# Performance work log

Hardware: AMD Instinct MI355X
Metric: run time of the kernel (lower is better)

The kernel has to match this reference:

```python
import jax, jax.numpy as jnp
import numpy as np

N, B, LMAX, DIM, IMG_DIM, LY, H = 32768, 16, 2560, 512, 768, 256, 8


def _layernorm(x, g, b, eps=1e-5):
    mu = jnp.mean(x, axis=-1, keepdims=True)
    var = jnp.mean(jnp.square(x - mu), axis=-1, keepdims=True)
    return (x - mu) * jax.lax.rsqrt(var + eps) * g + b


def setup_inputs() -> dict:
    key = jax.random.key(0)
    ks = jax.random.split(key, 16)
    s = DIM ** -0.5
    # ragged per-batch counts summing to N, all <= LMAX
    counts = np.full(B, N // B, dtype=np.int64)
    counts[: B // 2] += 200
    counts[B // 2:] -= 200
    batch_ids = jnp.asarray(np.repeat(np.arange(B), counts), dtype=jnp.int32)
    return {
        "F": jax.random.normal(ks[0], (N, DIM), jnp.float32),
        "y": jax.random.normal(ks[1], (B, LY, IMG_DIM), jnp.float32),
        "ln_g": jnp.ones((DIM,), jnp.float32),
        "ln_b": jnp.zeros((DIM,), jnp.float32),
        "Wq": jax.random.normal(ks[2], (DIM, DIM), jnp.float32) * s,
        "Wk": jax.random.normal(ks[3], (DIM, DIM), jnp.float32) * s,
        "Wv": jax.random.normal(ks[4], (DIM, DIM), jnp.float32) * s,
        "bq": jnp.zeros((DIM,), jnp.float32),
        "bk": jnp.zeros((DIM,), jnp.float32),
        "bv": jnp.zeros((DIM,), jnp.float32),
        "Wo": jax.random.normal(ks[5], (DIM, DIM), jnp.float32) * s,
        "bo": jnp.zeros((DIM,), jnp.float32),
        "W1": jax.random.normal(ks[6], (DIM, IMG_DIM), jnp.float32) * (IMG_DIM ** -0.5),
        "b1": jnp.zeros((DIM,), jnp.float32),
        "W2": jax.random.normal(ks[7], (DIM, DIM), jnp.float32) * s,
        "b2": jnp.zeros((DIM,), jnp.float32),
        "batch_ids": batch_ids,
        "Lmax": LMAX,
    }


def reference(F, y, ln_g, ln_b, Wq, Wk, Wv, bq, bk, bv, Wo, bo, W1, b1, W2, b2, batch_ids, Lmax):
    Bb, Ly, _ = y.shape
    n, dim = F.shape
    dh = dim // H
    # sparse -> dense: per-token slot index within its batch (batch_ids sorted)
    offsets = jnp.searchsorted(batch_ids, jnp.arange(Bb, dtype=batch_ids.dtype))
    pos = jnp.arange(n, dtype=jnp.int32) - offsets[batch_ids].astype(jnp.int32)
    xd = jnp.zeros((Bb, Lmax, dim), F.dtype).at[batch_ids, pos].set(F)  # [B,Lmax,D]
    # NOTE: self.norm is re-bound in subclass => same LayerNorm used twice
    xd = _layernorm(xd, ln_g, ln_b)
    # MLP fuse of image features: Linear -> GELU(exact) -> Linear
    ym = jax.nn.gelu(y @ W1.T + b1, approximate=False) @ W2.T + b2  # [B,Ly,D]
    # MHA cross-attention (no key_padding_mask: mask arg defaults to None)
    q = (xd @ Wq.T + bq).reshape(Bb, Lmax, H, dh)
    k = (ym @ Wk.T + bk).reshape(Bb, Ly, H, dh)
    v = (ym @ Wv.T + bv).reshape(Bb, Ly, H, dh)
    scores = jnp.einsum("bqhd,bkhd->bhqk", q, k) * (dh ** -0.5)
    attn = jax.nn.softmax(scores, axis=-1)
    o = jnp.einsum("bhqk,bkhd->bqhd", attn, v).reshape(Bb, Lmax, dim)
    o = o @ Wo.T + bo
    out_dense = _layernorm(xd + o, ln_g, ln_b)
    # dense -> sparse gather (equivalent to x_dense[x_mask])
    return out_dense[batch_ids, pos]
```

## Files before the change

### kernel.cpp

```cpp
#include <hip/hip_runtime.h>
#include <stdint.h>

#define NTOK 32768
#define BD   512
#define NB   16
#define LYK  256
#define IMGD 768

typedef __attribute__((ext_vector_type(4))) float f32x4;
typedef __attribute__((ext_vector_type(8))) short s16x8;
typedef __attribute__((ext_vector_type(4))) unsigned short u16x4;
typedef unsigned short u16;

__device__ __forceinline__ float bf2f(u16 u) {
  union { uint32_t i; float f; } v; v.i = ((uint32_t)u) << 16; return v.f;
}
__device__ __forceinline__ u16 f2bf(float f) {
  union { float f; uint32_t i; } v; v.f = f;
  uint32_t r = v.i + 0x7fffu + ((v.i >> 16) & 1u);
  return (u16)(r >> 16);
}
__device__ __forceinline__ u16 f2bf_fast(float f) {
  union { float f; uint32_t i; } v; v.f = f;
  return (u16)((v.i + 0x8000u) >> 16);
}
__device__ __forceinline__ void gl_lds16(const u16* g, u16* l) {
  __builtin_amdgcn_global_load_lds(
      (const __attribute__((address_space(1))) uint32_t*)g,
      (__attribute__((address_space(3))) uint32_t*)l, 16, 0, 0);
}
__device__ __forceinline__ f32x4 mfma16(s16x8 a, s16x8 b, f32x4 c) {
  return __builtin_amdgcn_mfma_f32_16x16x32_bf16(a, b, c, 0, 0, 0);
}

__global__ __launch_bounds__(256) void prep(
    const float* __restrict__ wq, const float* __restrict__ wk,
    const float* __restrict__ wv, const float* __restrict__ wo,
    const float* __restrict__ w2, const float* __restrict__ w1,
    const float* __restrict__ y,  const float* __restrict__ F,
    const float* __restrict__ g,  const float* __restrict__ be,
    const int* __restrict__ bids,
    u16* __restrict__ dq, u16* __restrict__ dkv, u16* __restrict__ dwo,
    u16* __restrict__ dw2, u16* __restrict__ dw1, u16* __restrict__ dy,
    u16* __restrict__ xn, int* __restrict__ off) {
  const int bid = blockIdx.x;
  if (bid < 2368) {
    const float* s; u16* d; int base;
    if      (bid < 128)  { s = wq; d = dq;            base = 0;   }
    else if (bid < 256)  { s = wk; d = dkv;           base = 128; }
    else if (bid < 384)  { s = wv; d = dkv + 262144;  base = 256; }
    else if (bid < 512)  { s = wo; d = dwo;           base = 384; }
    else if (bid < 640)  { s = w2; d = dw2;           base = 512; }
    else if (bid < 832)  { s = w1; d = dw1;           base = 640; }
    else                 { s = y;  d = dy;            base = 832; }
    int i = ((bid - base) * 256 + threadIdx.x) * 8;
    f32x4 a = *(const f32x4*)(s + i);
    f32x4 b = *(const f32x4*)(s + i + 4);
    s16x8 o;
#pragma unroll
    for (int j = 0; j < 4; ++j) { o[j] = (short)f2bf(a[j]); o[4 + j] = (short)f2bf(b[j]); }
    *(s16x8*)(d + i) = o;
  } else if (bid < 10560) {
    const int lane = threadIdx.x & 63;
    const size_t row = (size_t)(bid - 2368) * 4 + (threadIdx.x >> 6);
    const float* x = F + row * BD + lane * 8;
    f32x4 a = *(const f32x4*)x;
    f32x4 b = *(const f32x4*)(x + 4);
    float v[8] = {a[0], a[1], a[2], a[3], b[0], b[1], b[2], b[3]};
    float s = 0.f, s2 = 0.f;
#pragma unroll
    for (int j = 0; j < 8; ++j) { s += v[j]; s2 += v[j] * v[j]; }
#pragma unroll
    for (int m = 1; m < 64; m <<= 1) { s += __shfl_xor(s, m); s2 += __shfl_xor(s2, m); }
    float mean = s * (1.f / BD);
    float rstd = rsqrtf(s2 * (1.f / BD) - mean * mean + 1e-5f);
    const float* gp = g + lane * 8;
    const float* bp = be + lane * 8;
    s16x8 o;
#pragma unroll
    for (int j = 0; j < 8; ++j) o[j] = (short)f2bf((v[j] - mean) * rstd * gp[j] + bp[j]);
    *(s16x8*)(xn + row * BD + lane * 8) = o;
  } else {
    int b = threadIdx.x;
    if (b > NB) return;
    int lo = 0, hi = NTOK;
    while (lo < hi) { int mid = (lo + hi) >> 1; if (bids[mid] < b) lo = mid + 1; else hi = mid; }
    off[b] = lo;
  }
}

__global__ __launch_bounds__(256) void ln_bf16_f32(const u16* __restrict__ Z,
                                                   const float* __restrict__ g,
                                                   const float* __restrict__ be,
                                                   float* __restrict__ out) {
  const int lane = threadIdx.x & 63;
  const size_t row = (size_t)blockIdx.x * 4 + (threadIdx.x >> 6);
  s16x8 zv = *(const s16x8*)(Z + row * BD + lane * 8);
  float v[8];
#pragma unroll
  for (int j = 0; j < 8; ++j) v[j] = bf2f((u16)zv[j]);
  float s = 0.f, s2 = 0.f;
#pragma unroll
  for (int j = 0; j < 8; ++j) { s += v[j]; s2 += v[j] * v[j]; }
#pragma unroll
  for (int m = 1; m < 64; m <<= 1) { s += __shfl_xor(s, m); s2 += __shfl_xor(s2, m); }
  float mean = s * (1.f / BD);
  float rstd = rsqrtf(s2 * (1.f / BD) - mean * mean + 1e-5f);
  const float* gp = g + lane * 8;
  const float* bp = be + lane * 8;
  f32x4 o0, o1;
#pragma unroll
  for (int j = 0; j < 4; ++j) o0[j] = (v[j] - mean) * rstd * gp[j] + bp[j];
#pragma unroll
  for (int j = 0; j < 4; ++j) o1[j] = (v[4 + j] - mean) * rstd * gp[4 + j] + bp[4 + j];
  float* op = out + row * BD + lane * 8;
  *(f32x4*)op = o0;
  *(f32x4*)(op + 4) = o1;
}

template <int EPI>
__global__ __launch_bounds__(256, 2) void gemm64(const u16* __restrict__ A,
                                                 const u16* __restrict__ W,
                                                 const float* __restrict__ bias,
                                                 u16* __restrict__ C, int K) {
  __shared__ u16 As[64 * 32];
  __shared__ u16 Bs[128 * 32];
  const int tid = threadIdx.x;
  const int wave = tid >> 6, lane = tid & 63;
  const int wn = wave * 32;
  const int quad = lane >> 4, l16 = lane & 15;
  const int m0 = blockIdx.x * 64, n0 = blockIdx.y * 128;

  f32x4 acc[4][2];
#pragma unroll
  for (int i = 0; i < 4; ++i)
#pragma unroll
    for (int j = 0; j < 2; ++j) acc[i][j] = f32x4{0.f, 0.f, 0.f, 0.f};

  const int scol = (lane & 3) * 8;
  const u16* gA0 = A + (size_t)(m0 + wave * 16 + (lane >> 2)) * K + scol;
  const u16* gW0 = W + (size_t)(n0 + wave * 32 + (lane >> 2)) * K + scol;
  const u16* gW1 = gW0 + (size_t)16 * K;
  u16* lA = As + wave * 512;
  u16* lB = Bs + wave * 1024;

  for (int k0 = 0; k0 < K; k0 += 32) {
    __syncthreads();
    gl_lds16(gA0 + k0, lA);
    gl_lds16(gW0 + k0, lB);
    gl_lds16(gW1 + k0, lB + 512);
    __syncthreads();
    s16x8 af[4], bfr[2];
#pragma unroll
    for (int mt = 0; mt < 4; ++mt)
      af[mt] = *(const s16x8*)&As[(mt * 16 + l16) * 32 + quad * 8];
#pragma unroll
    for (int nt = 0; nt < 2; ++nt)
      bfr[nt] = *(const s16x8*)&Bs[(wn + nt * 16 + l16) * 32 + quad * 8];
#pragma unroll
    for (int mt = 0; mt < 4; ++mt)
#pragma unroll
      for (int nt = 0; nt < 2; ++nt)
        acc[mt][nt] = mfma16(af[mt], bfr[nt], acc[mt][nt]);
  }

#pragma unroll
  for (int nt = 0; nt < 2; ++nt) {
    const int n = n0 + wn + nt * 16 + l16;
    const float bia = bias[n];
#pragma unroll
    for (int mt = 0; mt < 4; ++mt) {
      const int mb = m0 + mt * 16 + quad * 4;
#pragma unroll
      for (int r = 0; r < 4; ++r) {
        float v = acc[mt][nt][r] + bia;
        if (EPI == 1) v = 0.5f * v * (1.f + erff(v * 0.70710678118654752f));
        C[(size_t)(mb + r) * BD + n] = f2bf(v);
      }
    }
  }
}

template <int EPI, int SWZ>
__global__ __launch_bounds__(256, 2) void gemm128(const u16* __restrict__ A,
                                                  const u16* __restrict__ W,
                                                  const float* __restrict__ bias,
                                                  u16* __restrict__ C,
                                                  const u16* __restrict__ resid,
                                                  u16* __restrict__ C2,
                                                  const float* __restrict__ bias2,
                                                  int K) {
  __shared__ u16 As[2][128 * 32];
  __shared__ u16 Bs[2][128 * 32];
  const int tid = threadIdx.x;
  const int wave = tid >> 6, lane = tid & 63;
  const int wm = (wave & 1) * 64, wn = (wave >> 1) * 64;
  const int quad = lane >> 4, l16 = lane & 15;
  int m_t, n_t;
  if (SWZ) {
    const int bid = blockIdx.x;
    const int xcd = bid & 7, j = bid >> 3;
    n_t = j & 3;
    m_t = xcd + (j >> 2) * 8;
  } else {
    m_t = blockIdx.x; n_t = blockIdx.y;
  }
  const int m0 = m_t * 128, n0 = n_t * 128;

  f32x4 acc[4][4];
#pragma unroll
  for (int i = 0; i < 4; ++i)
#pragma unroll
    for (int j = 0; j < 4; ++j) acc[i][j] = f32x4{0.f, 0.f, 0.f, 0.f};

  const int srow = wave * 32 + (lane >> 2);
  const int scol = (lane & 3) * 8;
  const u16* gA0 = A + (size_t)(m0 + srow) * K + scol;
  const u16* gA1 = gA0 + (size_t)16 * K;
  const u16* gW0 = W + (size_t)(n0 + srow) * K + scol;
  const u16* gW1 = gW0 + (size_t)16 * K;
  const int wb = wave * 1024;

  gl_lds16(gA0, &As[0][wb]);
  gl_lds16(gA1, &As[0][wb + 512]);
  gl_lds16(gW0, &Bs[0][wb]);
  gl_lds16(gW1, &Bs[0][wb + 512]);

  int buf = 0;
  for (int k0 = 0; k0 < K; k0 += 32, buf ^= 1) {
    __syncthreads();
    if (k0 + 32 < K) {
      const int nb = buf ^ 1, k1 = k0 + 32;
      gl_lds16(gA0 + k1, &As[nb][wb]);
      gl_lds16(gA1 + k1, &As[nb][wb + 512]);
      gl_lds16(gW0 + k1, &Bs[nb][wb]);
      gl_lds16(gW1 + k1, &Bs[nb][wb + 512]);
    }
    s16x8 af[4], bfr[4];
#pragma unroll
    for (int mt = 0; mt < 4; ++mt)
      af[mt] = *(const s16x8*)&As[buf][(wm + mt * 16 + l16) * 32 + quad * 8];
#pragma unroll
    for (int nt = 0; nt < 4; ++nt)
      bfr[nt] = *(const s16x8*)&Bs[buf][(wn + nt * 16 + l16) * 32 + quad * 8];
#pragma unroll
    for (int mt = 0; mt < 4; ++mt)
#pragma unroll
      for (int nt = 0; nt < 4; ++nt)
        acc[mt][nt] = mfma16(af[mt], bfr[nt], acc[mt][nt]);
  }

#pragma unroll
  for (int nt = 0; nt < 4; ++nt) {
    const int n = n0 + wn + nt * 16 + l16;
    const float bia = (EPI == 3) ? (n < BD ? bias[n] : bias2[n - BD]) : bias[n];
#pragma unroll
    for (int mt = 0; mt < 4; ++mt) {
      const int mb = m0 + wm + mt * 16 + quad * 4;
      if (EPI == 3 && n >= BD) {
        u16x4 pk;
#pragma unroll
        for (int r = 0; r < 4; ++r) pk[r] = f2bf(acc[mt][nt][r] + bia);
        const int b = mb >> 8, k0i = mb & 255;
        *(u16x4*)&C2[((size_t)b * BD + (n - BD)) * LYK + k0i] = pk;
      } else {
#pragma unroll
        for (int r = 0; r < 4; ++r) {
          float v = acc[mt][nt][r] + bia;
          size_t idx = (size_t)(mb + r) * BD + n;
          if (EPI == 2) v += bf2f(resid[idx]);
          C[idx] = f2bf(v);
        }
      }
    }
  }
}

__global__ __launch_bounds__(256, 2) void attn_k(const u16* __restrict__ Q,
                                                 const u16* __restrict__ Kg,
                                                 const u16* __restrict__ VT,
                                                 const int* __restrict__ off,
                                                 u16* __restrict__ O) {
  const int t = blockIdx.x, h = blockIdx.y, b = blockIdx.z;
  const int qend = off[b + 1];
  const int qstart = off[b] + t * 64;
  if (qstart >= qend) return;

  __shared__ u16 KT[256 * 72];
  __shared__ u16 VTs[64 * 264];

  const int tid = threadIdx.x;
  const int wave = tid >> 6, lane = tid & 63;
  const int quad = lane >> 4, l16 = lane & 15;

  {
    const u16* src = Kg + (size_t)b * LYK * BD + h * 64;
#pragma unroll
    for (int s = 0; s < 8; ++s) {
      int c = tid + s * 256;
      int r = c >> 3, col = (c & 7) * 8;
      *(s16x8*)&KT[r * 72 + col] = *(const s16x8*)&src[(size_t)r * BD + col];
    }
  }
  {
    const u16* src = VT + ((size_t)b * BD + h * 64) * LYK;
#pragma unroll
    for (int s = 0; s < 8; ++s) {
      int c = tid + s * 256;
      int r = c >> 5, col = (c & 31) * 8;
      *(s16x8*)&VTs[r * 264 + col] = *(const s16x8*)&src[(size_t)r * LYK + col];
    }
  }
  int qrow = qstart + wave * 16 + l16;
  if (qrow > NTOK - 1) qrow = NTOK - 1;
  const u16* qp = Q + (size_t)qrow * BD + h * 64 + quad * 8;
  s16x8 aq0 = *(const s16x8*)qp;
  s16x8 aq1 = *(const s16x8*)(qp + 32);

  __syncthreads();

  f32x4 sacc[16];
#pragma unroll
  for (int nt = 0; nt < 16; ++nt) sacc[nt] = f32x4{0.f, 0.f, 0.f, 0.f};
#pragma unroll
  for (int nt = 0; nt < 16; ++nt) {
    const u16* kp = &KT[(nt * 16 + l16) * 72 + quad * 8];
    s16x8 k0 = *(const s16x8*)kp;
    s16x8 k1 = *(const s16x8*)(kp + 32);
    sacc[nt] = mfma16(k0, aq0, sacc[nt]);
    sacc[nt] = mfma16(k1, aq1, sacc[nt]);
  }

  float mx = -1e30f;
#pragma unroll
  for (int nt = 0; nt < 16; ++nt)
#pragma unroll
    for (int r = 0; r < 4; ++r) mx = fmaxf(mx, sacc[nt][r]);
  mx = fmaxf(mx, __shfl_xor(mx, 16));
  mx = fmaxf(mx, __shfl_xor(mx, 32));
  float sum = 0.f;
#pragma unroll
  for (int nt = 0; nt < 16; ++nt)
#pragma unroll
    for (int r = 0; r < 4; ++r) {
      float p = __expf(0.125f * (sacc[nt][r] - mx));
      sacc[nt][r] = p;
      sum += p;
    }
  sum += __shfl_xor(sum, 16);
  sum += __shfl_xor(sum, 32);
  const float inv = 1.f / sum;

  __syncthreads();

  u16* P = KT;
  const int prow = (wave * 16 + l16) * 264;
#pragma unroll
  for (int nt = 0; nt < 16; ++nt) {
    u16x4 pk;
#pragma unroll
    for (int r = 0; r < 4; ++r) pk[r] = f2bf_fast(sacc[nt][r] * inv);
    *(u16x4*)&P[prow + nt * 16 + quad * 4] = pk;
  }

  f32x4 oacc[4];
#pragma unroll
  for (int n2 = 0; n2 < 4; ++n2) oacc[n2] = f32x4{0.f, 0.f, 0.f, 0.f};
#pragma unroll
  for (int kc = 0; kc < 8; ++kc) {
    s16x8 ap = *(const s16x8*)&P[prow + kc * 32 + quad * 8];
#pragma unroll
    for (int n2 = 0; n2 < 4; ++n2) {
      s16x8 bv = *(const s16x8*)&VTs[(n2 * 16 + l16) * 264 + kc * 32 + quad * 8];
      oacc[n2] = mfma16(ap, bv, oacc[n2]);
    }
  }

#pragma unroll
  for (int n2 = 0; n2 < 4; ++n2)
#pragma unroll
    for (int r = 0; r < 4; ++r) {
      int q = qstart + wave * 16 + quad * 4 + r;
      if (q < qend)
        O[(size_t)q * BD + h * 64 + n2 * 16 + l16] = f2bf(oacc[n2][r]);
    }
}

extern "C" void kernel_launch(void* const* d_in, const int* in_sizes, int n_in,
                              void* d_out, int out_size, void* d_ws, size_t ws_size,
                              hipStream_t stream) {
  const float* F    = (const float*)d_in[0];
  const float* yIn  = (const float*)d_in[1];
  const float* ln_g = (const float*)d_in[2];
  const float* ln_b = (const float*)d_in[3];
  const float* Wq   = (const float*)d_in[4];
  const float* Wk   = (const float*)d_in[5];
  const float* Wv   = (const float*)d_in[6];
  const float* bq   = (const float*)d_in[7];
  const float* bk   = (const float*)d_in[8];
  const float* bv   = (const float*)d_in[9];
  const float* Wo   = (const float*)d_in[10];
  const float* bo   = (const float*)d_in[11];
  const float* W1   = (const float*)d_in[12];
  const float* b1   = (const float*)d_in[13];
  const float* W2   = (const float*)d_in[14];
  const float* b2   = (const float*)d_in[15];
  const int* bids   = (const int*)d_in[16];

  char* ws = (char*)d_ws;
  size_t cur = 0;
  auto alloc = [&](size_t bytes) {
    void* p = ws + cur;
    cur += (bytes + 255) & ~(size_t)255;
    return p;
  };

  int* off   = (int*)alloc(68);
  u16* wq_b  = (u16*)alloc((size_t)262144 * 2);
  u16* wkv_b = (u16*)alloc((size_t)524288 * 2);
  u16* wo_b  = (u16*)alloc((size_t)262144 * 2);
  u16* w2_b  = (u16*)alloc((size_t)262144 * 2);
  u16* w1_b  = (u16*)alloc((size_t)393216 * 2);
  u16* y_b   = (u16*)alloc((size_t)3145728 * 2);
  u16* U     = (u16*)alloc((size_t)4096 * BD * 2);
  u16* ym    = (u16*)alloc((size_t)4096 * BD * 2);
  u16* Kb    = (u16*)alloc((size_t)4096 * BD * 2);
  u16* VT    = (u16*)alloc((size_t)NB * BD * LYK * 2);
  u16* xn    = (u16*)alloc((size_t)NTOK * BD * 2);
  u16* Qb    = (u16*)alloc((size_t)NTOK * BD * 2);
  u16* Ob    = (u16*)alloc((size_t)NTOK * BD * 2);
  u16* Zb    = (u16*)alloc((size_t)NTOK * BD * 2);

  prep<<<10561, 256, 0, stream>>>(Wq, Wk, Wv, Wo, W2, W1, yIn, F, ln_g, ln_b, bids,
                                  wq_b, wkv_b, wo_b, w2_b, w1_b, y_b, xn, off);

  gemm64<1><<<dim3(64, 4), 256, 0, stream>>>(y_b, w1_b, b1, U, IMGD);
  gemm64<0><<<dim3(64, 4), 256, 0, stream>>>(U, w2_b, b2, ym, BD);
  gemm128<3, 0><<<dim3(32, 8), 256, 0, stream>>>(ym, wkv_b, bk, Kb, nullptr, VT, bv, BD);
  gemm128<0, 1><<<1024, 256, 0, stream>>>(xn, wq_b, bq, Qb, nullptr, nullptr, nullptr, BD);
  attn_k<<<dim3(36, 8, NB), 256, 0, stream>>>(Qb, Kb, VT, off, Ob);
  gemm128<2, 1><<<1024, 256, 0, stream>>>(Ob, wo_b, bo, Zb, xn, nullptr, nullptr, BD);
  ln_bf16_f32<<<NTOK / 4, 256, 0, stream>>>(Zb, ln_g, ln_b, (float*)d_out);
}
```

Before: 335.4 us.

## Make attention persistent per (batch, head) with swizzled async LDS loads

The attention kernel moves from one 256-thread block per 64-query tile to 512 persistent 512-thread blocks, each owning a batch/head slice and looping over 128-query tiles. K and V are loaded into LDS once per block via global_load_lds with XOR swizzling, which removes the repeated K/V reloads and padded layouts. Softmax now uses exp2 with a fused scale, packed bf16 conversion, and normalisation deferred to the output. The block-ID remap spreads work across XCDs, but the fixed 4 tiles per head could leave load imbalance across the ragged batches.

After: 339.8 us. About the same (+1.3%).

```diff
diff --git a/kernel.cpp b/kernel.cpp
--- a/kernel.cpp
+++ b/kernel.cpp
@@ -31,6 +31,11 @@
 }
 __device__ __forceinline__ f32x4 mfma16(s16x8 a, s16x8 b, f32x4 c) {
   return __builtin_amdgcn_mfma_f32_16x16x32_bf16(a, b, c, 0, 0, 0);
+}
+__device__ __forceinline__ uint32_t cvtpk(float a, float b) {
+  uint32_t r;
+  asm("v_cvt_pk_bf16_f32 %0, %1, %2" : "=v"(r) : "v"(a), "v"(b));
+  return r;
 }
 
 __global__ __launch_bounds__(256) void prep(
@@ -276,114 +281,136 @@
   }
 }
 
-__global__ __launch_bounds__(256, 2) void attn_k(const u16* __restrict__ Q,
+__global__ __launch_bounds__(512, 1) void attn_k(const u16* __restrict__ Q,
                                                  const u16* __restrict__ Kg,
                                                  const u16* __restrict__ VT,
                                                  const int* __restrict__ off,
                                                  u16* __restrict__ O) {
-  const int t = blockIdx.x, h = blockIdx.y, b = blockIdx.z;
-  const int qend = off[b + 1];
-  const int qstart = off[b] + t * 64;
-  if (qstart >= qend) return;
-
-  __shared__ u16 KT[256 * 72];
-  __shared__ u16 VTs[64 * 264];
+  const int bid = blockIdx.x;
+  const int lin = (bid & 7) * 64 + (bid >> 3);
+  const int t = lin & 3;
+  const int h = (lin >> 2) & 7;
+  const int b = lin >> 5;
+
+  __shared__ u16 KS[256 * 64];
+  __shared__ u16 VS[64 * 256];
+  __shared__ u16 P[128 * 264];
 
   const int tid = threadIdx.x;
   const int wave = tid >> 6, lane = tid & 63;
   const int quad = lane >> 4, l16 = lane & 15;
 
   {
-    const u16* src = Kg + (size_t)b * LYK * BD + h * 64;
-#pragma unroll
-    for (int s = 0; s < 8; ++s) {
-      int c = tid + s * 256;
-      int r = c >> 3, col = (c & 7) * 8;
-      *(s16x8*)&KT[r * 72 + col] = *(const s16x8*)&src[(size_t)r * BD + col];
-    }
-  }
-  {
-    const u16* src = VT + ((size_t)b * BD + h * 64) * LYK;
-#pragma unroll
-    for (int s = 0; s < 8; ++s) {
-      int c = tid + s * 256;
-      int r = c >> 5, col = (c & 31) * 8;
-      *(s16x8*)&VTs[r * 264 + col] = *(const s16x8*)&src[(size_t)r * LYK + col];
-    }
-  }
-  int qrow = qstart + wave * 16 + l16;
-  if (qrow > NTOK - 1) qrow = NTOK - 1;
-  const u16* qp = Q + (size_t)qrow * BD + h * 64 + quad * 8;
-  s16x8 aq0 = *(const s16x8*)qp;
-  s16x8 aq1 = *(const s16x8*)(qp + 32);
-
+    const int c8 = lane & 7, r8 = lane >> 3;
+    const u16* kbase = Kg + (size_t)(b * LYK) * BD + h * 64 + ((c8 ^ r8) << 3);
+#pragma unroll
+    for (int j = 0; j < 4; ++j) {
+      const int blk = wave * 4 + j;
+      gl_lds16(kbase + (size_t)(blk * 8 + r8) * BD, KS + blk * 512);
+    }
+    const int c32 = lane & 31, r2 = lane >> 5;
+#pragma unroll
+    for (int j = 0; j < 4; ++j) {
+      const int blk = wave * 4 + j;
+      const int r = blk * 2 + r2;
+      gl_lds16(VT + (size_t)(b * BD + h * 64 + r) * LYK + ((c32 ^ (r & 31)) << 3),
+               VS + blk * 512);
+    }
+  }
   __syncthreads();
 
-  f32x4 sacc[16];
-#pragma unroll
-  for (int nt = 0; nt < 16; ++nt) sacc[nt] = f32x4{0.f, 0.f, 0.f, 0.f};
-#pragma unroll
-  for (int nt = 0; nt < 16; ++nt) {
-    const u16* kp = &KT[(nt * 16 + l16) * 72 + quad * 8];
-    s16x8 k0 = *(const s16x8*)kp;
-    s16x8 k1 = *(const s16x8*)(kp + 32);
-    sacc[nt] = mfma16(k0, aq0, sacc[nt]);
-    sacc[nt] = mfma16(k1, aq1, sacc[nt]);
-  }
-
-  float mx = -1e30f;
-#pragma unroll
-  for (int nt = 0; nt < 16; ++nt)
-#pragma unroll
-    for (int r = 0; r < 4; ++r) mx = fmaxf(mx, sacc[nt][r]);
-  mx = fmaxf(mx, __shfl_xor(mx, 16));
-  mx = fmaxf(mx, __shfl_xor(mx, 32));
-  float sum = 0.f;
-#pragma unroll
-  for (int nt = 0; nt < 16; ++nt)
-#pragma unroll
-    for (int r = 0; r < 4; ++r) {
-      float p = __expf(0.125f * (sacc[nt][r] - mx));
-      sacc[nt][r] = p;
-      sum += p;
-    }
-  sum += __shfl_xor(sum, 16);
-  sum += __shfl_xor(sum, 32);
-  const float inv = 1.f / sum;
-
-  __syncthreads();
-
-  u16* P = KT;
+  const int qbase = off[b], qend = off[b + 1];
+  const int kc0 = ((quad ^ (l16 & 7)) << 3);
+  const int kc1 = (((quad + 4) ^ (l16 & 7)) << 3);
   const int prow = (wave * 16 + l16) * 264;
-#pragma unroll
-  for (int nt = 0; nt < 16; ++nt) {
-    u16x4 pk;
-#pragma unroll
-    for (int r = 0; r < 4; ++r) pk[r] = f2bf_fast(sacc[nt][r] * inv);
-    *(u16x4*)&P[prow + nt * 16 + quad * 4] = pk;
-  }
-
-  f32x4 oacc[4];
-#pragma unroll
-  for (int n2 = 0; n2 < 4; ++n2) oacc[n2] = f32x4{0.f, 0.f, 0.f, 0.f};
-#pragma unroll
-  for (int kc = 0; kc < 8; ++kc) {
-    s16x8 ap = *(const s16x8*)&P[prow + kc * 32 + quad * 8];
-#pragma unroll
-    for (int n2 = 0; n2 < 4; ++n2) {
-      s16x8 bv = *(const s16x8*)&VTs[(n2 * 16 + l16) * 264 + kc * 32 + quad * 8];
-      oacc[n2] = mfma16(ap, bv, oacc[n2]);
-    }
-  }
-
-#pragma unroll
-  for (int n2 = 0; n2 < 4; ++n2)
-#pragma unroll
-    for (int r = 0; r < 4; ++r) {
-      int q = qstart + wave * 16 + quad * 4 + r;
-      if (q < qend)
-        O[(size_t)q * BD + h * 64 + n2 * 16 + l16] = f2bf(oacc[n2][r]);
-    }
+  int vbase[4], vm[4];
+#pragma unroll
+  for (int n2 = 0; n2 < 4; ++n2) {
+    const int rv = n2 * 16 + l16;
+    vbase[n2] = rv * 256;
+    vm[n2] = (rv & 31) << 3;
+  }
+
+  for (int it = t;; it += 4) {
+    const int q0 = qbase + it * 128;
+    if (q0 >= qend) break;
+    const int qw = q0 + wave * 16;
+    if (qw >= qend) continue;
+    int qrow = qw + l16;
+    if (qrow > qend - 1) qrow = qend - 1;
+    const u16* qp = Q + (size_t)qrow * BD + h * 64 + quad * 8;
+    const s16x8 aq0 = *(const s16x8*)qp;
+    const s16x8 aq1 = *(const s16x8*)(qp + 32);
+
+    f32x4 sacc[16];
+#pragma unroll
+    for (int nt = 0; nt < 16; ++nt) sacc[nt] = f32x4{0.f, 0.f, 0.f, 0.f};
+#pragma unroll
+    for (int nt = 0; nt < 16; ++nt) {
+      const u16* kp = &KS[(nt * 16 + l16) * 64];
+      const s16x8 k0 = *(const s16x8*)(kp + kc0);
+      const s16x8 k1 = *(const s16x8*)(kp + kc1);
+      sacc[nt] = mfma16(k0, aq0, sacc[nt]);
+      sacc[nt] = mfma16(k1, aq1, sacc[nt]);
+    }
+
+    f32x4 m4 = sacc[0];
+#pragma unroll
+    for (int nt = 1; nt < 16; ++nt)
+#pragma unroll
+      for (int r = 0; r < 4; ++r) m4[r] = fmaxf(m4[r], sacc[nt][r]);
+    float mx = fmaxf(fmaxf(m4[0], m4[1]), fmaxf(m4[2], m4[3]));
+    mx = fmaxf(mx, __shfl_xor(mx, 16));
+    mx = fmaxf(mx, __shfl_xor(mx, 32));
+    const float c1 = 0.18033688011112042f;
+    const float mc = -mx * c1;
+    f32x4 s4 = f32x4{0.f, 0.f, 0.f, 0.f};
+#pragma unroll
+    for (int nt = 0; nt < 16; ++nt)
+#pragma unroll
+      for (int r = 0; r < 4; ++r) {
+        const float p = __builtin_exp2f(fmaf(sacc[nt][r], c1, mc));
+        sacc[nt][r] = p;
+        s4[r] += p;
+      }
+    float sum = (s4[0] + s4[1]) + (s4[2] + s4[3]);
+    sum += __shfl_xor(sum, 16);
+    sum += __shfl_xor(sum, 32);
+    const float inv = 1.f / sum;
+
+#pragma unroll
+    for (int nt = 0; nt < 16; ++nt) {
+      uint2 pk;
+      pk.x = cvtpk(sacc[nt][0], sacc[nt][1]);
+      pk.y = cvtpk(sacc[nt][2], sacc[nt][3]);
+      *(uint2*)&P[prow + nt * 16 + quad * 4] = pk;
+    }
+
+    f32x4 oacc[4];
+#pragma unroll
+    for (int n2 = 0; n2 < 4; ++n2) oacc[n2] = f32x4{0.f, 0.f, 0.f, 0.f};
+#pragma unroll
+    for (int kc = 0; kc < 8; ++kc) {
+      const s16x8 ap = *(const s16x8*)&P[prow + kc * 32 + quad * 8];
+#pragma unroll
+      for (int n2 = 0; n2 < 4; ++n2) {
+        const s16x8 bv = *(const s16x8*)&VS[vbase[n2] + ((kc * 32 + quad * 8) ^ vm[n2])];
+        oacc[n2] = mfma16(ap, bv, oacc[n2]);
+      }
+    }
+
+    float invr[4];
+#pragma unroll
+    for (int r = 0; r < 4; ++r) invr[r] = __shfl(inv, quad * 4 + r);
+#pragma unroll
+    for (int n2 = 0; n2 < 4; ++n2)
+#pragma unroll
+      for (int r = 0; r < 4; ++r) {
+        const int q = qw + quad * 4 + r;
+        if (q < qend)
+          O[(size_t)q * BD + h * 64 + n2 * 16 + l16] = f2bf(oacc[n2][r] * invr[r]);
+      }
+  }
 }
 
 extern "C" void kernel_launch(void* const* d_in, const int* in_sizes, int n_in,
@@ -438,7 +465,7 @@
   gemm64<0><<<dim3(64, 4), 256, 0, stream>>>(U, w2_b, b2, ym, BD);
   gemm128<3, 0><<<dim3(32, 8), 256, 0, stream>>>(ym, wkv_b, bk, Kb, nullptr, VT, bv, BD);
   gemm128<0, 1><<<1024, 256, 0, stream>>>(xn, wq_b, bq, Qb, nullptr, nullptr, nullptr, BD);
-  attn_k<<<dim3(36, 8, NB), 256, 0, stream>>>(Qb, Kb, VT, off, Ob);
+  attn_k<<<512, 512, 0, stream>>>(Qb, Kb, VT, off, Ob);
   gemm128<2, 1><<<1024, 256, 0, stream>>>(Ob, wo_b, bo, Zb, xn, nullptr, nullptr, BD);
   ln_bf16_f32<<<NTOK / 4, 256, 0, stream>>>(Zb, ln_g, ln_b, (float*)d_out);
 }
```
